# Kernel tuning notes

Hardware: AMD Instinct MI355X
Metric: run time of the kernel (lower is better)

Reference implementation:

```python
import jax, jax.numpy as jnp
import numpy as np
from jax import lax

NUM_HEADS = 8


def setup_inputs() -> dict:
    key = jax.random.key(0)
    ks = jax.random.split(key, 6)
    B, L, Hd = 4, 4096, 512
    S = 45  # factor * ceil(ln(L)) = 5 * 9
    x = jax.random.normal(ks[0], (B, L, Hd), dtype=jnp.float32)
    scale = 1.0 / np.sqrt(Hd)
    Wq = jax.random.normal(ks[1], (Hd, Hd), dtype=jnp.float32) * scale
    Wk = jax.random.normal(ks[2], (Hd, Hd), dtype=jnp.float32) * scale
    Wv = jax.random.normal(ks[3], (Hd, Hd), dtype=jnp.float32) * scale
    Wo = jax.random.normal(ks[4], (Hd, Hd), dtype=jnp.float32) * scale
    index_sample = jax.random.randint(ks[5], (L, S), 0, L, dtype=jnp.int32)
    return {"x": x, "Wq": Wq, "Wk": Wk, "Wv": Wv, "Wo": Wo,
            "index_sample": index_sample}


def reference(x, Wq, Wk, Wv, Wo, index_sample):
    B, L, Hd = x.shape
    H = NUM_HEADS
    D = Hd // H
    S = index_sample.shape[1]
    u = S  # n_top active queries = factor*ceil(ln(L))

    def split_heads(t):  # [B,L,Hd] -> [B,H,L,D]
        return t.reshape(B, L, H, D).transpose(0, 2, 1, 3)

    q = split_heads(x @ Wq)
    k = split_heads(x @ Wk)
    v = split_heads(x @ Wv)

    scale = 1.0 / jnp.sqrt(jnp.asarray(D, dtype=x.dtype))

    # sampled key gather: [B,H,L,S,D]
    K_samp = k[:, :, index_sample, :]
    # sampled scores per query: [B,H,L,S]
    QK_samp = jnp.einsum('bhld,bhlsd->bhls', q, K_samp)
    # sparsity measurement: max - mean over sampled keys
    M = QK_samp.max(axis=-1) - QK_samp.mean(axis=-1)  # [B,H,L]
    _, top_idx = lax.top_k(M, u)                      # [B,H,u]

    # full attention only for active queries
    Qr = jnp.take_along_axis(q, top_idx[..., None], axis=2)   # [B,H,u,D]
    scores = jnp.einsum('bhud,bhld->bhul', Qr, k) * scale     # [B,H,u,L]
    attn = jax.nn.softmax(scores, axis=-1)
    ctx_sel = jnp.einsum('bhul,bhld->bhud', attn, v)          # [B,H,u,D]

    # inactive queries get mean(V); scatter active results in
    context = jnp.broadcast_to(v.mean(axis=2, keepdims=True), (B, H, L, D))
    b_idx = jnp.arange(B)[:, None, None]
    h_idx = jnp.arange(H)[None, :, None]
    context = context.at[b_idx, h_idx, top_idx].set(ctx_sel)

    out = context.transpose(0, 2, 1, 3).reshape(B, L, Hd) @ Wo
    return out
```

## Files before the change

### kernel.cpp

```cpp
#include <hip/hip_runtime.h>
#include <cmath>

#define SS 45
#define FSPLIT 16

typedef __attribute__((ext_vector_type(8))) _Float16 half8;
typedef __attribute__((ext_vector_type(4))) float float4v;

__device__ inline unsigned short f16b(float f) {
    union { _Float16 h; unsigned short u; } c;
    c.h = (_Float16)f;
    return c.u;
}
__device__ inline float f16back(unsigned short u) {
    union { _Float16 h; unsigned short u; } c;
    c.u = u;
    return (float)c.h;
}

__device__ __forceinline__ void async16(const void* g, void* l) {
    __builtin_amdgcn_global_load_lds(
        (const __attribute__((address_space(1))) void*)g,
        (__attribute__((address_space(3))) void*)l, 16, 0, 0);
}

template <int CTRL>
__device__ __forceinline__ float dppadd(float v) {
    int x = __builtin_amdgcn_mov_dpp(__float_as_int(v), CTRL, 0xF, 0xF, true);
    return v + __int_as_float(x);
}
template <int CTRL>
__device__ __forceinline__ float dppmax(float v) {
    int x = __builtin_amdgcn_mov_dpp(__float_as_int(v), CTRL, 0xF, 0xF, true);
    return fmaxf(v, __int_as_float(x));
}

__device__ __forceinline__ unsigned int fmono(float f) {
    unsigned int u = __float_as_uint(f);
    return (u & 0x80000000u) ? ~u : (u | 0x80000000u);
}

__global__ __launch_bounds__(256) void conv_kernel(
    const float4* __restrict__ x4, ushort4* __restrict__ xh4, ushort4* __restrict__ xl4,
    const float* __restrict__ Wq, const float* __restrict__ Wk, const float* __restrict__ Wv,
    unsigned short* __restrict__ WTh, unsigned short* __restrict__ WTl,
    float* __restrict__ vmp)
{
    int bid = blockIdx.x;
    if (bid < 8192) {
        int i = bid * 256 + threadIdx.x;
        float4 v = x4[i];
        float fv[4] = {v.x, v.y, v.z, v.w};
        ushort4 h, l;
        unsigned short hh[4], ll[4];
        #pragma unroll
        for (int e = 0; e < 4; e++) {
            hh[e] = f16b(fv[e]);
            ll[e] = f16b(fv[e] - f16back(hh[e]));
        }
        h.x = hh[0]; h.y = hh[1]; h.z = hh[2]; h.w = hh[3];
        l.x = ll[0]; l.y = ll[1]; l.z = ll[2]; l.w = ll[3];
        xh4[i] = h; xl4[i] = l;
    } else if (bid < 8960) {
        int wb = bid - 8192;
        int zy = wb >> 8;
        int bxy = wb & 255;
        const float* W = (zy == 0) ? Wq : (zy == 1) ? Wk : Wv;
        unsigned short* th = WTh + (size_t)zy * 262144;
        unsigned short* tl = WTl + (size_t)zy * 262144;
        __shared__ float t[32][33];
        int bx = bxy & 15, by = bxy >> 4;
        int tx = threadIdx.x & 31, ty = threadIdx.x >> 5;
        for (int i = ty; i < 32; i += 8) t[i][tx] = W[(size_t)(by * 32 + i) * 512 + bx * 32 + tx];
        __syncthreads();
        for (int i = ty; i < 32; i += 8) {
            float f = t[tx][i];
            unsigned short h = f16b(f);
            unsigned short lo = f16b(f - f16back(h));
            th[(size_t)(bx * 32 + i) * 512 + by * 32 + tx] = h;
            tl[(size_t)(bx * 32 + i) * 512 + by * 32 + tx] = lo;
        }
    } else {
        for (int i = threadIdx.x; i < 2048; i += 256) vmp[i] = 0.f;
    }
}

__global__ __launch_bounds__(512, 2) void qkv6_kernel(
    const unsigned short* __restrict__ Xh, const unsigned short* __restrict__ Xl,
    const unsigned short* __restrict__ WTh, const unsigned short* __restrict__ WTl,
    float* __restrict__ Q, float* __restrict__ K, float* __restrict__ V,
    float* __restrict__ vmp)
{
    __shared__ unsigned short lds[73728];

    int wave = threadIdx.x >> 6;
    int lane = threadIdx.x & 63;
    int m0blk = blockIdx.x * 256;
    int n0blk = blockIdx.y * 128;
    int fr = lane & 15;
    int C = lane >> 4;
    int srow = lane >> 2;
    int sslot = lane & 3;
    int mrb = (wave >> 1) * 64;
    int nrb = (wave & 1) * 64;

    const unsigned short* gb[7];
    gb[0] = Xh;
    gb[1] = Xl;
    gb[2] = WTh;
    gb[3] = WTl;
    gb[4] = WTh + 262144;
    gb[5] = WTl + 262144;
    gb[6] = WTh + 524288;

    float4v accq[4][4], acck[4][4], accv[4][4];
    #pragma unroll
    for (int i = 0; i < 4; i++)
        #pragma unroll
        for (int j = 0; j < 4; j++) {
            accq[i][j] = (float4v){0.f, 0.f, 0.f, 0.f};
            acck[i][j] = (float4v){0.f, 0.f, 0.f, 0.f};
            accv[i][j] = (float4v){0.f, 0.f, 0.f, 0.f};
        }

    auto stage = [&](int buf, int k0) {
        #pragma unroll
        for (int t = 0; t < 2; t++)
            #pragma unroll
            for (int inst = 0; inst < 2; inst++) {
                int rloc = wave * 32 + inst * 16 + srow;
                int Cp = sslot ^ ((rloc >> 1) & 3);
                const unsigned short* g = gb[t] + (size_t)(m0blk + rloc) * 512 + k0 + Cp * 8;
                async16(g, lds + buf * 36864 + t * 8192 + (wave * 32 + inst * 16) * 32);
            }
        #pragma unroll
        for (int t = 2; t < 7; t++) {
            int rloc = wave * 16 + srow;
            int Cp = sslot ^ ((rloc >> 1) & 3);
            const unsigned short* g = gb[t] + (size_t)(n0blk + rloc) * 512 + k0 + Cp * 8;
            async16(g, lds + buf * 36864 + 16384 + (t - 2) * 4096 + wave * 512);
        }
    };

    stage(0, 0);

    for (int kk = 0; kk < 16; kk++) {
        const unsigned short* Lb = lds + (kk & 1) * 36864;
        if (kk < 15) {
            stage((kk + 1) & 1, (kk + 1) * 32);
            asm volatile("s_waitcnt vmcnt(9)" ::: "memory");
        } else {
            asm volatile("s_waitcnt vmcnt(0)" ::: "memory");
        }
        __builtin_amdgcn_s_barrier();

        half8 A_h[4], A_l[4];
        #pragma unroll
        for (int i = 0; i < 4; i++) {
            int R = mrb + i * 16 + fr;
            int sl = C ^ ((R >> 1) & 3);
            A_h[i] = *(const half8*)(Lb + R * 32 + sl * 8);
            A_l[i] = *(const half8*)(Lb + 8192 + R * 32 + sl * 8);
        }
        #pragma unroll
        for (int j = 0; j < 4; j++) {
            int R = nrb + j * 16 + fr;
            int sl = C ^ ((R >> 1) & 3);
            int off = R * 32 + sl * 8;
            half8 Bqh = *(const half8*)(Lb + 16384 + off);
            half8 Bql = *(const half8*)(Lb + 20480 + off);
            half8 Bkh = *(const half8*)(Lb + 24576 + off);
            half8 Bkl = *(const half8*)(Lb + 28672 + off);
            half8 Bvh = *(const half8*)(Lb + 32768 + off);
            #pragma unroll
            for (int i = 0; i < 4; i++) {
                accq[i][j] = __builtin_amdgcn_mfma_f32_16x16x32_f16(A_h[i], Bqh, accq[i][j], 0, 0, 0);
                accq[i][j] = __builtin_amdgcn_mfma_f32_16x16x32_f16(A_h[i], Bql, accq[i][j], 0, 0, 0);
                accq[i][j] = __builtin_amdgcn_mfma_f32_16x16x32_f16(A_l[i], Bqh, accq[i][j], 0, 0, 0);
                acck[i][j] = __builtin_amdgcn_mfma_f32_16x16x32_f16(A_h[i], Bkh, acck[i][j], 0, 0, 0);
                acck[i][j] = __builtin_amdgcn_mfma_f32_16x16x32_f16(A_h[i], Bkl, acck[i][j], 0, 0, 0);
                acck[i][j] = __builtin_amdgcn_mfma_f32_16x16x32_f16(A_l[i], Bkh, acck[i][j], 0, 0, 0);
                accv[i][j] = __builtin_amdgcn_mfma_f32_16x16x32_f16(A_h[i], Bvh, accv[i][j], 0, 0, 0);
            }
        }
        __builtin_amdgcn_s_barrier();
    }

    int hh = n0blk + nrb;
    int hd = hh >> 6;
    int bb0 = (m0blk + mrb) >> 12;
    {
        float cs[4];
        #pragma unroll
        for (int j = 0; j < 4; j++) {
            float s = 0.f;
            #pragma unroll
            for (int i = 0; i < 4; i++)
                #pragma unroll
                for (int r = 0; r < 4; r++) s += accv[i][j][r];
            s += __shfl_xor(s, 16, 64);
            s += __shfl_xor(s, 32, 64);
            cs[j] = s;
        }
        if (C == 0) {
            #pragma unroll
            for (int j = 0; j < 4; j++)
                atomicAdd(vmp + ((size_t)(bb0 * 8 + hd) * 64) + j * 16 + fr, cs[j]);
        }
    }

    int rbase = C * 4;
    int m0 = m0blk + mrb;
    #pragma unroll
    for (int i = 0; i < 4; i++)
        #pragma unroll
        for (int r = 0; r < 4; r++) {
            int rg = m0 + i * 16 + rbase + r;
            int bb = rg >> 12, l = rg & 4095;
            size_t rowoff = ((size_t)(bb * 8 + hd) * 4096 + l) * 64;
            #pragma unroll
            for (int j = 0; j < 4; j++) Q[rowoff + j * 16 + fr] = accq[i][j][r];
            #pragma unroll
            for (int j = 0; j < 4; j++) K[rowoff + j * 16 + fr] = acck[i][j][r];
            #pragma unroll
            for (int j = 0; j < 4; j++) V[rowoff + j * 16 + fr] = accv[i][j][r];
        }
}

__global__ __launch_bounds__(256) void m_kernel(
    const float* __restrict__ Q, const float* __restrict__ K,
    const int* __restrict__ idx, float* __restrict__ M)
{
    int inst = blockIdx.x * 4 + (threadIdx.x >> 6);
    int lane = threadIdx.x & 63;
    int g = lane >> 3;
    int t = lane & 7;
    int bh = inst >> 12;
    int l = inst & 4095;
    float4 qa = *(const float4*)(Q + (size_t)inst * 64 + t * 4);
    float4 qb = *(const float4*)(Q + (size_t)inst * 64 + 32 + t * 4);
    const float* kb = K + (size_t)bh * 4096 * 64;
    const int* irow = idx + (size_t)l * SS;
    int jv[6];
    #pragma unroll
    for (int it = 0; it < 6; it++) {
        int s = it * 8 + g;
        jv[it] = irow[(it == 5 && g >= 5) ? 0 : s];
    }
    float4 kva[6], kvb[6];
    #pragma unroll
    for (int it = 0; it < 6; it++) {
        kva[it] = *(const float4*)(kb + (size_t)jv[it] * 64 + t * 4);
        kvb[it] = *(const float4*)(kb + (size_t)jv[it] * 64 + 32 + t * 4);
    }
    float maxv = -1e30f, sum = 0.f, p0 = 0.f;
    #pragma unroll
    for (int it = 0; it < 6; it++) {
        float p = qa.x * kva[it].x;
        p = fmaf(qa.y, kva[it].y, p);
        p = fmaf(qa.z, kva[it].z, p);
        p = fmaf(qa.w, kva[it].w, p);
        p = fmaf(qb.x, kvb[it].x, p);
        p = fmaf(qb.y, kvb[it].y, p);
        p = fmaf(qb.z, kvb[it].z, p);
        p = fmaf(qb.w, kvb[it].w, p);
        p = dppadd<0xB1>(p);
        p = dppadd<0x4E>(p);
        p = dppadd<0x141>(p);
        if (it == 0) p0 = p;
        maxv = fmaxf(maxv, p);
        sum += p;
    }
    maxv = dppmax<0x128>(maxv);
    maxv = fmaxf(maxv, __shfl_xor(maxv, 16, 64));
    maxv = fmaxf(maxv, __shfl_xor(maxv, 32, 64));
    sum = dppadd<0x128>(sum);
    sum += __shfl_xor(sum, 16, 64);
    sum += __shfl_xor(sum, 32, 64);
    float p0b = __shfl(p0, 0, 64);
    if (lane == 0) M[inst] = maxv - (sum - 3.f * p0b) * (1.f / 45.f);
}

__global__ __launch_bounds__(256) void topk_local_kernel(
    const float* __restrict__ M, unsigned long long* __restrict__ cand)
{
    int chunk = blockIdx.x;
    int bh = chunk >> 3, c = chunk & 7;
    __shared__ unsigned long long keys[512];
    int tid = threadIdx.x;
    for (int i = tid; i < 512; i += 256) {
        int l = c * 512 + i;
        unsigned int u = fmono(M[(size_t)bh * 4096 + l]);
        keys[i] = ((unsigned long long)u << 32) | (unsigned int)(4095 - l);
    }
    __syncthreads();
    for (int k = 2; k <= 512; k <<= 1)
        for (int j = k >> 1; j > 0; j >>= 1) {
            for (int i0 = tid; i0 < 512; i0 += 256) {
                int ixj = i0 ^ j;
                if (ixj > i0) {
                    unsigned long long a = keys[i0], b = keys[ixj];
                    bool asc = (i0 & k) != 0;
                    if (asc ? (a > b) : (a < b)) { keys[i0] = b; keys[ixj] = a; }
                }
            }
            __syncthreads();
        }
    if (tid < SS) cand[(size_t)chunk * SS + tid] = keys[tid];
}

__global__ __launch_bounds__(256) void topk_merge_base_kernel(
    const unsigned long long* __restrict__ cand, int* __restrict__ tidx,
    const float* __restrict__ vmp, const float* __restrict__ Wo,
    float* __restrict__ vmean, float* __restrict__ base)
{
    int bid = blockIdx.x;
    int tid = threadIdx.x;
    if (bid < 32) {
        __shared__ unsigned long long keys[512];
        for (int i = tid; i < 512; i += 256) {
            unsigned long long v = 0ull;
            if (i < 8 * SS) {
                int cc = i / SS, r = i - cc * SS;
                v = cand[((size_t)bid * 8 + cc) * SS + r];
            }
            keys[i] = v;
        }
        __syncthreads();
        for (int k = 2; k <= 512; k <<= 1)
            for (int j = k >> 1; j > 0; j >>= 1) {
                for (int i0 = tid; i0 < 512; i0 += 256) {
                    int ixj = i0 ^ j;
                    if (ixj > i0) {
                        unsigned long long a = keys[i0], b = keys[ixj];
                        bool asc = (i0 & k) != 0;
                        if (asc ? (a > b) : (a < b)) { keys[i0] = b; keys[ixj] = a; }
                    }
                }
                __syncthreads();
            }
        if (tid < SS) tidx[bid * SS + tid] = 4095 - (int)(keys[tid] & 0xFFFFFFFFu);
    } else {
        int b = bid - 32;
        __shared__ float vmS[512];
        for (int i = tid; i < 512; i += 256) {
            float s = vmp[(size_t)b * 512 + i] * (1.f / 4096.f);
            vmS[i] = s;
            vmean[(size_t)b * 512 + i] = s;
        }
        __syncthreads();
        for (int jj = tid; jj < 512; jj += 256) {
            float s = 0.f;
            for (int i = 0; i < 512; i++) s += vmS[i] * Wo[(size_t)i * 512 + jj];
            base[(size_t)b * 512 + jj] = s;
        }
    }
}

__global__ __launch_bounds__(256) void attn_fill_kernel(
    const float* __restrict__ Q, const float* __restrict__ K, const float* __restrict__ V,
    const int* __restrict__ tidx,
    float* __restrict__ Opart, float* __restrict__ mpart, float* __restrict__ lpart,
    const float4* __restrict__ base4, float4* __restrict__ out4)
{
    int bid = blockIdx.x;
    if (bid >= 512) {
        int i = (bid - 512) * 256 + threadIdx.x;
        int b = i >> 19;
        int j4 = i & 127;
        out4[i] = base4[b * 128 + j4];
        return;
    }
    int split = bid & 15;
    int bh = bid >> 4;
    int L0 = split * (4096 / FSPLIT);

    __shared__ float Qs[48][68];
    __shared__ float Ks[64][68];
    __shared__ float Vs[64][68];
    __shared__ float Ps[48][68];
    __shared__ int tS[48];

    int tid = threadIdx.x;
    int lane = tid & 63, w = tid >> 6;
    if (tid < 48) tS[tid] = (tid < SS) ? tidx[bh * SS + tid] : 0;
    __syncthreads();
    for (int u = w; u < 48; u += 4)
        Qs[u][lane] = Q[((size_t)bh * 4096 + tS[u]) * 64 + lane];

    int ug = tid >> 4, lg = tid & 15;
    float mrun[4], lrun[4], O[4][4];
    #pragma unroll
    for (int i = 0; i < 4; i++) {
        mrun[i] = -1e30f; lrun[i] = 0.f;
        #pragma unroll
        for (int j = 0; j < 4; j++) O[i][j] = 0.f;
    }

    for (int tt = 0; tt < 4096 / FSPLIT / 64; tt++) {
        int lbase = L0 + tt * 64;
        if (tt > 0) __syncthreads();
        for (int r = w; r < 64; r += 4) {
            Ks[r][lane] = K[((size_t)bh * 4096 + lbase + r) * 64 + lane];
            Vs[r][lane] = V[((size_t)bh * 4096 + lbase + r) * 64 + lane];
        }
        __syncthreads();

        if (tid < 192) {
            float acc[4][4];
            #pragma unroll
            for (int i = 0; i < 4; i++)
                #pragma unroll
                for (int j = 0; j < 4; j++) acc[i][j] = 0.f;
            for (int d0 = 0; d0 < 64; d0 += 4) {
                float4 a[4], b[4];
                #pragma unroll
                for (int i = 0; i < 4; i++) a[i] = *(float4*)&Qs[ug * 4 + i][d0];
                #pragma unroll
                for (int j = 0; j < 4; j++) b[j] = *(float4*)&Ks[lg * 4 + j][d0];
                #pragma unroll
                for (int i = 0; i < 4; i++)
                    #pragma unroll
                    for (int j = 0; j < 4; j++)
                        acc[i][j] += a[i].x * b[j].x + a[i].y * b[j].y + a[i].z * b[j].z + a[i].w * b[j].w;
            }
            #pragma unroll
            for (int i = 0; i < 4; i++) {
                #pragma unroll
                for (int j = 0; j < 4; j++) acc[i][j] *= 0.125f;
                float tm = fmaxf(fmaxf(acc[i][0], acc[i][1]), fmaxf(acc[i][2], acc[i][3]));
                tm = fmaxf(tm, __shfl_xor(tm, 1, 64));
                tm = fmaxf(tm, __shfl_xor(tm, 2, 64));
                tm = fmaxf(tm, __shfl_xor(tm, 4, 64));
                tm = fmaxf(tm, __shfl_xor(tm, 8, 64));
                float nm = fmaxf(mrun[i], tm);
                float corr = __expf(mrun[i] - nm);
                float rs = 0.f;
                #pragma unroll
                for (int j = 0; j < 4; j++) {
                    float p = __expf(acc[i][j] - nm);
                    Ps[ug * 4 + i][lg * 4 + j] = p;
                    rs += p;
                }
                rs += __shfl_xor(rs, 1, 64);
                rs += __shfl_xor(rs, 2, 64);
                rs += __shfl_xor(rs, 4, 64);
                rs += __shfl_xor(rs, 8, 64);
                lrun[i] = lrun[i] * corr + rs;
                mrun[i] = nm;
                #pragma unroll
                for (int j = 0; j < 4; j++) O[i][j] *= corr;
            }
        }
        __syncthreads();

        if (tid < 192) {
            for (int l0 = 0; l0 < 64; l0 += 4) {
                float4 vr[4];
                #pragma unroll
                for (int r = 0; r < 4; r++) vr[r] = *(float4*)&Vs[l0 + r][lg * 4];
                #pragma unroll
                for (int i = 0; i < 4; i++) {
                    float4 pv = *(float4*)&Ps[ug * 4 + i][l0];
                    #pragma unroll
                    for (int j = 0; j < 4; j++) {
                        float vj0 = (&vr[0].x)[j], vj1 = (&vr[1].x)[j];
                        float vj2 = (&vr[2].x)[j], vj3 = (&vr[3].x)[j];
                        O[i][j] = fmaf(pv.x, vj0, fmaf(pv.y, vj1, fmaf(pv.z, vj2, fmaf(pv.w, vj3, O[i][j]))));
                    }
                }
            }
        }
    }

    if (tid < 192) {
        #pragma unroll
        for (int i = 0; i < 4; i++) {
            int u = ug * 4 + i;
            if (u < SS) {
                size_t pbase = ((size_t)(bh * FSPLIT + split) * SS + u);
                if (lg == 0) { mpart[pbase] = mrun[i]; lpart[pbase] = lrun[i]; }
                #pragma unroll
                for (int j = 0; j < 4; j++)
                    Opart[pbase * 64 + lg * 4 + j] = O[i][j];
            }
        }
    }
}

__global__ __launch_bounds__(256) void combine_kernel(
    const float* __restrict__ Opart, const float* __restrict__ mpart, const float* __restrict__ lpart,
    const float* __restrict__ vmean, const float* __restrict__ Wo,
    const int* __restrict__ tidx, float* __restrict__ out)
{
    int rr = blockIdx.x;
    int bh = rr / SS, u = rr % SS;
    int h = bh & 7, b = bh >> 3;
    __shared__ float dS[64];
    int tid = threadIdx.x;
    if (tid < 64) {
        float m = -1e30f;
        #pragma unroll
        for (int s = 0; s < FSPLIT; s++)
            m = fmaxf(m, mpart[(size_t)(bh * FSPLIT + s) * SS + u]);
        float den = 0.f, num = 0.f;
        #pragma unroll
        for (int s = 0; s < FSPLIT; s++) {
            size_t pbase = (size_t)(bh * FSPLIT + s) * SS + u;
            float wgt = __expf(mpart[pbase] - m);
            den += wgt * lpart[pbase];
            num += wgt * Opart[pbase * 64 + tid];
        }
        dS[tid] = num / den - vmean[(size_t)bh * 64 + tid];
    }
    __syncthreads();
    int l = tidx[rr];
    float* orow = out + ((size_t)b * 4096 + l) * 512;
    for (int j = tid; j < 512; j += 256) {
        float s = 0.f;
        #pragma unroll
        for (int dd = 0; dd < 64; dd++) s += dS[dd] * Wo[(size_t)(h * 64 + dd) * 512 + j];
        atomicAdd(orow + j, s);
    }
}

extern "C" void kernel_launch(void* const* d_in, const int* in_sizes, int n_in,
                              void* d_out, int out_size, void* d_ws, size_t ws_size,
                              hipStream_t stream)
{
    const float* x  = (const float*)d_in[0];
    const float* Wq = (const float*)d_in[1];
    const float* Wk = (const float*)d_in[2];
    const float* Wv = (const float*)d_in[3];
    const float* Wo = (const float*)d_in[4];
    const int*  idx = (const int*)d_in[5];
    float* out = (float*)d_out;

    float* W = (float*)d_ws;
    float* Q = W;
    float* K = W + 8388608;
    float* V = W + 16777216;
    unsigned short* xh  = (unsigned short*)(W + 25165824);
    unsigned short* xl  = (unsigned short*)(W + 29360128);
    unsigned short* WTh = (unsigned short*)(W + 33554432);
    unsigned short* WTl = (unsigned short*)(W + 33947648);
    float* vmp = W + 34340864;

    float* Mv    = W + 25165824;
    float* Opart = W + 25296896;
    float* mpart = W + 26771456;
    float* lpart = W + 26794496;
    float* vmean = W + 33439744;
    float* base  = W + 33441792;
    int*   tidx  = (int*)(W + 33443840);
    unsigned long long* cand = (unsigned long long*)(W + 33445280);

    conv_kernel<<<8961, 256, 0, stream>>>((const float4*)x, (ushort4*)xh, (ushort4*)xl,
                                          Wq, Wk, Wv, WTh, WTl, vmp);
    qkv6_kernel<<<dim3(64, 4), 512, 0, stream>>>(xh, xl, WTh, WTl, Q, K, V, vmp);
    m_kernel<<<32768, 256, 0, stream>>>(Q, K, idx, Mv);
    topk_local_kernel<<<256, 256, 0, stream>>>(Mv, cand);
    topk_merge_base_kernel<<<36, 256, 0, stream>>>(cand, tidx, vmp, Wo, vmean, base);
    attn_fill_kernel<<<512 + 8192, 256, 0, stream>>>(Q, K, V, tidx, Opart, mpart, lpart,
                                                     (const float4*)base, (float4*)out);
    combine_kernel<<<1440, 256, 0, stream>>>(Opart, mpart, lpart, vmean, Wo, tidx, out);
}
```

Baseline: 408.8 us.

## Fuse x fp16 hi/lo split into QKV GEMM A-tile staging

Drops the separate conversion pass that split x into fp16 high and low arrays in global memory. The QKV GEMM now loads fp32 x tiles into registers, splits them into hi/lo in-kernel, and writes them to LDS, while the weight tiles still use async global-to-LDS loads. This removes a full write and re-read of the converted activations, at the cost of register-staged A loads and a full vmcnt(0) wait before each barrier, which can expose load latency in the pipeline.

```diff
diff --git a/kernel.cpp b/kernel.cpp
--- a/kernel.cpp
+++ b/kernel.cpp
@@ -6,6 +6,7 @@
 
 typedef __attribute__((ext_vector_type(8))) _Float16 half8;
 typedef __attribute__((ext_vector_type(4))) float float4v;
+typedef __attribute__((ext_vector_type(8))) unsigned short ushort8v;
 
 __device__ inline unsigned short f16b(float f) {
     union { _Float16 h; unsigned short u; } c;
@@ -40,31 +41,15 @@
     return (u & 0x80000000u) ? ~u : (u | 0x80000000u);
 }
 
-__global__ __launch_bounds__(256) void conv_kernel(
-    const float4* __restrict__ x4, ushort4* __restrict__ xh4, ushort4* __restrict__ xl4,
+__global__ __launch_bounds__(256) void convW_kernel(
     const float* __restrict__ Wq, const float* __restrict__ Wk, const float* __restrict__ Wv,
     unsigned short* __restrict__ WTh, unsigned short* __restrict__ WTl,
     float* __restrict__ vmp)
 {
     int bid = blockIdx.x;
-    if (bid < 8192) {
-        int i = bid * 256 + threadIdx.x;
-        float4 v = x4[i];
-        float fv[4] = {v.x, v.y, v.z, v.w};
-        ushort4 h, l;
-        unsigned short hh[4], ll[4];
-        #pragma unroll
-        for (int e = 0; e < 4; e++) {
-            hh[e] = f16b(fv[e]);
-            ll[e] = f16b(fv[e] - f16back(hh[e]));
-        }
-        h.x = hh[0]; h.y = hh[1]; h.z = hh[2]; h.w = hh[3];
-        l.x = ll[0]; l.y = ll[1]; l.z = ll[2]; l.w = ll[3];
-        xh4[i] = h; xl4[i] = l;
-    } else if (bid < 8960) {
-        int wb = bid - 8192;
-        int zy = wb >> 8;
-        int bxy = wb & 255;
+    if (bid < 768) {
+        int zy = bid >> 8;
+        int bxy = bid & 255;
         const float* W = (zy == 0) ? Wq : (zy == 1) ? Wk : Wv;
         unsigned short* th = WTh + (size_t)zy * 262144;
         unsigned short* tl = WTl + (size_t)zy * 262144;
@@ -85,8 +70,8 @@
     }
 }
 
-__global__ __launch_bounds__(512, 2) void qkv6_kernel(
-    const unsigned short* __restrict__ Xh, const unsigned short* __restrict__ Xl,
+__global__ __launch_bounds__(512, 2) void qkv8_kernel(
+    const float* __restrict__ X,
     const unsigned short* __restrict__ WTh, const unsigned short* __restrict__ WTl,
     float* __restrict__ Q, float* __restrict__ K, float* __restrict__ V,
     float* __restrict__ vmp)
@@ -104,14 +89,19 @@
     int mrb = (wave >> 1) * 64;
     int nrb = (wave & 1) * 64;
 
-    const unsigned short* gb[7];
-    gb[0] = Xh;
-    gb[1] = Xl;
-    gb[2] = WTh;
-    gb[3] = WTl;
-    gb[4] = WTh + 262144;
-    gb[5] = WTl + 262144;
-    gb[6] = WTh + 524288;
+    const unsigned short* gbB[5];
+    gbB[0] = WTh;
+    gbB[1] = WTl;
+    gbB[2] = WTh + 262144;
+    gbB[3] = WTl + 262144;
+    gbB[4] = WTh + 524288;
+
+    int rloc0 = wave * 32 + srow;
+    int rloc1 = wave * 32 + 16 + srow;
+    int Cp0 = sslot ^ ((rloc0 >> 1) & 3);
+    int Cp1 = sslot ^ ((rloc1 >> 1) & 3);
+    const float* xr0 = X + (size_t)(m0blk + rloc0) * 512 + Cp0 * 8;
+    const float* xr1 = X + (size_t)(m0blk + rloc1) * 512 + Cp1 * 8;
 
     float4v accq[4][4], acck[4][4], accv[4][4];
     #pragma unroll
@@ -123,36 +113,56 @@
             accv[i][j] = (float4v){0.f, 0.f, 0.f, 0.f};
         }
 
-    auto stage = [&](int buf, int k0) {
-        #pragma unroll
-        for (int t = 0; t < 2; t++)
-            #pragma unroll
-            for (int inst = 0; inst < 2; inst++) {
-                int rloc = wave * 32 + inst * 16 + srow;
-                int Cp = sslot ^ ((rloc >> 1) & 3);
-                const unsigned short* g = gb[t] + (size_t)(m0blk + rloc) * 512 + k0 + Cp * 8;
-                async16(g, lds + buf * 36864 + t * 8192 + (wave * 32 + inst * 16) * 32);
-            }
-        #pragma unroll
-        for (int t = 2; t < 7; t++) {
-            int rloc = wave * 16 + srow;
-            int Cp = sslot ^ ((rloc >> 1) & 3);
-            const unsigned short* g = gb[t] + (size_t)(n0blk + rloc) * 512 + k0 + Cp * 8;
-            async16(g, lds + buf * 36864 + 16384 + (t - 2) * 4096 + wave * 512);
+    auto stageB = [&](int buf, int k0) {
+        int rloc = wave * 16 + srow;
+        int Cp = sslot ^ ((rloc >> 1) & 3);
+        #pragma unroll
+        for (int t = 0; t < 5; t++) {
+            const unsigned short* g = gbB[t] + (size_t)(n0blk + rloc) * 512 + k0 + Cp * 8;
+            async16(g, lds + buf * 36864 + 16384 + t * 4096 + wave * 512);
         }
     };
 
-    stage(0, 0);
+    float4 xv[2][2];
+    auto loadX = [&](int k0) {
+        xv[0][0] = *(const float4*)(xr0 + k0);
+        xv[0][1] = *(const float4*)(xr0 + k0 + 4);
+        xv[1][0] = *(const float4*)(xr1 + k0);
+        xv[1][1] = *(const float4*)(xr1 + k0 + 4);
+    };
+    auto writeA = [&](int buf) {
+        #pragma unroll
+        for (int inst = 0; inst < 2; inst++) {
+            const float* f = (const float*)&xv[inst][0];
+            ushort8v hv, lv;
+            #pragma unroll
+            for (int e = 0; e < 8; e++) {
+                unsigned short h = f16b(f[e]);
+                hv[e] = h;
+                lv[e] = f16b(f[e] - f16back(h));
+            }
+            unsigned short* dsth = lds + buf * 36864 + (wave * 32 + inst * 16) * 32 + lane * 8;
+            *(ushort8v*)dsth = hv;
+            *(ushort8v*)(dsth + 8192) = lv;
+        }
+    };
+
+    loadX(0);
+    stageB(0, 0);
+    writeA(0);
+    asm volatile("s_waitcnt vmcnt(0)" ::: "memory");
+    asm volatile("s_waitcnt lgkmcnt(0)" ::: "memory");
+    __builtin_amdgcn_s_barrier();
 
     for (int kk = 0; kk < 16; kk++) {
         const unsigned short* Lb = lds + (kk & 1) * 36864;
+        int nbuf = (kk + 1) & 1;
+        int nk0 = (kk + 1) * 32;
+
         if (kk < 15) {
-            stage((kk + 1) & 1, (kk + 1) * 32);
-            asm volatile("s_waitcnt vmcnt(9)" ::: "memory");
-        } else {
-            asm volatile("s_waitcnt vmcnt(0)" ::: "memory");
-        }
-        __builtin_amdgcn_s_barrier();
+            loadX(nk0);
+            stageB(nbuf, nk0);
+        }
 
         half8 A_h[4], A_l[4];
         #pragma unroll
@@ -183,7 +193,13 @@
                 accv[i][j] = __builtin_amdgcn_mfma_f32_16x16x32_f16(A_h[i], Bvh, accv[i][j], 0, 0, 0);
             }
         }
-        __builtin_amdgcn_s_barrier();
+
+        if (kk < 15) {
+            writeA(nbuf);
+            asm volatile("s_waitcnt vmcnt(0)" ::: "memory");
+            asm volatile("s_waitcnt lgkmcnt(0)" ::: "memory");
+            __builtin_amdgcn_s_barrier();
+        }
     }
 
     int hh = n0blk + nrb;
@@ -540,8 +556,6 @@
     float* Q = W;
     float* K = W + 8388608;
     float* V = W + 16777216;
-    unsigned short* xh  = (unsigned short*)(W + 25165824);
-    unsigned short* xl  = (unsigned short*)(W + 29360128);
     unsigned short* WTh = (unsigned short*)(W + 33554432);
     unsigned short* WTl = (unsigned short*)(W + 33947648);
     float* vmp = W + 34340864;
@@ -555,9 +569,8 @@
     int*   tidx  = (int*)(W + 33443840);
     unsigned long long* cand = (unsigned long long*)(W + 33445280);
 
-    conv_kernel<<<8961, 256, 0, stream>>>((const float4*)x, (ushort4*)xh, (ushort4*)xl,
-                                          Wq, Wk, Wv, WTh, WTl, vmp);
-    qkv6_kernel<<<dim3(64, 4), 512, 0, stream>>>(xh, xl, WTh, WTl, Q, K, V, vmp);
+    convW_kernel<<<769, 256, 0, stream>>>(Wq, Wk, Wv, WTh, WTl, vmp);
+    qkv8_kernel<<<dim3(64, 4), 512, 0, stream>>>(x, WTh, WTl, Q, K, V, vmp);
     m_kernel<<<32768, 256, 0, stream>>>(Q, K, idx, Mv);
     topk_local_kernel<<<256, 256, 0, stream>>>(Mv, cand);
     topk_merge_base_kernel<<<36, 256, 0, stream>>>(cand, tidx, vmp, Wo, vmean, base);
```

Result: faster. 399.7 us (-2.2%).
